# Kernel optimization log

Hardware: AMD Instinct MI355X
Metric: run time of the kernel (lower is better)

## Reference

```python
import jax, jax.numpy as jnp
import numpy as np

N = 50000
E = 800000
IN_C = 128
HEADS = 2
OUT_C = 64
NEG_SLOPE = 0.2  # PyG GATConv leaky_relu slope


def setup_inputs() -> dict:
    key = jax.random.key(0)
    ks = jax.random.split(key, 12)
    glorot = lambda k, shape: jax.random.normal(k, shape, jnp.float32) * np.sqrt(2.0 / (shape[0] + shape[-1]))
    return {
        "node_h": jax.random.normal(ks[0], (N, IN_C), jnp.float32),
        "edge_index_pc": jax.random.randint(ks[1], (2, E), 0, N, jnp.int64),
        "edge_index_mc": jax.random.randint(ks[2], (2, E), 0, N, jnp.int64),
        "W_pc": glorot(ks[3], (IN_C, HEADS * OUT_C)),
        "att_src_pc": glorot(ks[4], (HEADS, OUT_C)),
        "att_dst_pc": glorot(ks[5], (HEADS, OUT_C)),
        "bias_pc": jnp.zeros((HEADS * OUT_C,), jnp.float32),
        "W_mc": glorot(ks[6], (IN_C, HEADS * OUT_C)),
        "att_src_mc": glorot(ks[7], (HEADS, OUT_C)),
        "att_dst_mc": glorot(ks[8], (HEADS, OUT_C)),
        "bias_mc": jnp.zeros((HEADS * OUT_C,), jnp.float32),
    }


def _gat_conv(x, edge_index, W, att_src, att_dst, bias):
    # PyG GATConv (concat=True). x: [N, in], edge_index: [2, E] (src -> dst).
    n = x.shape[0]
    H, C = att_src.shape
    xw = (x @ W).reshape(n, H, C)                      # [N, H, C]
    a_src = jnp.sum(xw * att_src, axis=-1)             # [N, H]
    a_dst = jnp.sum(xw * att_dst, axis=-1)             # [N, H]
    src, dst = edge_index[0], edge_index[1]
    e = jax.nn.leaky_relu(a_src[src] + a_dst[dst], negative_slope=NEG_SLOPE)  # [E, H]
    # segment softmax over edges sharing the same destination node
    m = jax.ops.segment_max(e, dst, num_segments=n)    # [N, H]
    m = jnp.where(jnp.isfinite(m), m, 0.0)             # guard isolated nodes
    ex = jnp.exp(e - m[dst])
    denom = jax.ops.segment_sum(ex, dst, num_segments=n)
    alpha = ex / (denom[dst] + 1e-16)                  # [E, H]
    msg = xw[src] * alpha[:, :, None]                  # [E, H, C]
    out = jax.ops.segment_sum(msg, dst, num_segments=n)  # [N, H, C]
    return out.reshape(n, H * C) + bias


def reference(node_h, edge_index_pc, edge_index_mc,
              W_pc, att_src_pc, att_dst_pc, bias_pc,
              W_mc, att_src_mc, att_dst_mc, bias_mc):
    # eval mode: F.dropout and GATConv attention dropout are identity
    h_pc = jax.nn.elu(_gat_conv(node_h, edge_index_pc, W_pc, att_src_pc, att_dst_pc, bias_pc))
    h_mc = jax.nn.elu(_gat_conv(node_h, edge_index_mc, W_mc, att_src_mc, att_dst_mc, bias_mc))
    return (h_pc + h_mc) * 0.5
```

## Files before the change

### kernel.cpp

```cpp
#include <hip/hip_runtime.h>
#include <hip/hip_bf16.h>

#define IN_C   128
#define HC     128
#define OUT_C  64
#define EPB    4096
#define NBMAX  1024
#define CAP    4096

typedef short bf16x8 __attribute__((ext_vector_type(8)));
typedef float f32x4  __attribute__((ext_vector_type(4)));

__device__ __forceinline__ unsigned short f2bf(float f) {
    unsigned u = __float_as_uint(f);
    return (unsigned short)((u + 0x7FFF + ((u >> 16) & 1)) >> 16);
}

__device__ __forceinline__ void fma8(float* acc, float al, uint4 v) {
    acc[0] += al * __uint_as_float(v.x << 16);
    acc[1] += al * __uint_as_float(v.x & 0xFFFF0000u);
    acc[2] += al * __uint_as_float(v.y << 16);
    acc[3] += al * __uint_as_float(v.y & 0xFFFF0000u);
    acc[4] += al * __uint_as_float(v.z << 16);
    acc[5] += al * __uint_as_float(v.z & 0xFFFF0000u);
    acc[6] += al * __uint_as_float(v.w << 16);
    acc[7] += al * __uint_as_float(v.w & 0xFFFF0000u);
}

__global__ void k_detect(const void* __restrict__ h,
                         const void* __restrict__ e1,
                         const void* __restrict__ e2,
                         int* __restrict__ flags)
{
    if (blockIdx.x == 0 && threadIdx.x == 0) {
        const unsigned short* u = (const unsigned short*)h;
        int f32 = 0;
        for (int k = 0; k < 512; ++k) {
            int ex = (u[k] >> 7) & 0xFF;
            if (ex >= 0xE0) { f32 = 1; break; }
        }
        flags[0] = f32;
        const int* a = (const int*)e1;
        const int* b = (const int*)e2;
        int any1 = 0, any2 = 0;
        for (int k = 0; k < 64; ++k) { any1 |= a[2*k+1]; any2 |= b[2*k+1]; }
        flags[1] = (any1 == 0);
        flags[2] = (any2 == 0);
        flags[3] = 0;
    }
}

__device__ __forceinline__ float ldf(const void* p, int i, int f32) {
    if (f32) return ((const float*)p)[i];
    return __bfloat162float(((const __hip_bfloat16*)p)[i]);
}

__device__ __forceinline__ void load_edge(const void* ei, int e, int E, int i64,
                                          int& s, int& d)
{
    if (i64) {
        s = (int)((const long long*)ei)[e];
        d = (int)((const long long*)ei)[E + e];
    } else {
        s = ((const int*)ei)[e];
        d = ((const int*)ei)[E + e];
    }
}

__global__ void k_fill_sentinel(float* out, int total, float v)
{
    int i = blockIdx.x * blockDim.x + threadIdx.x;
    if (i < total) out[i] = v;
}

__global__ __launch_bounds__(256)
void k_prep(const void* __restrict__ Wpc, const void* __restrict__ Wmc,
            const int* __restrict__ flags,
            unsigned short* __restrict__ WTpc, unsigned short* __restrict__ WTmc)
{
    int idx = blockIdx.x * 256 + threadIdx.x;
    if (idx >= 2 * IN_C * HC) return;
    int conv = idx >= IN_C * HC;
    int r = idx - conv * IN_C * HC;
    int k = r >> 7, j = r & 127;
    float v = ldf(conv ? Wmc : Wpc, r, flags[0]);
    (conv ? WTmc : WTpc)[(size_t)j * IN_C + k] = f2bf(v);
}

__global__ __launch_bounds__(256)
void k_gs(const void* __restrict__ h,
          const unsigned short* __restrict__ WT0,
          const unsigned short* __restrict__ WT1,
          const void* __restrict__ atS0, const void* __restrict__ atD0,
          const void* __restrict__ atS1, const void* __restrict__ atD1,
          const int* __restrict__ flags,
          unsigned short* __restrict__ xw0, unsigned short* __restrict__ xw1,
          float* __restrict__ oas0, float* __restrict__ oad0,
          float* __restrict__ oas1, float* __restrict__ oad1,
          int n, int blocksG,
          const void* __restrict__ e1, const void* __restrict__ e2, int E,
          int NB, int blocksB,
          int* __restrict__ gcur1, int* __restrict__ gcur2,
          unsigned* __restrict__ bkt1, unsigned* __restrict__ bkt2)
{
    __shared__ int sh[2 * NBMAX];
    int tid = threadIdx.x;

    if (blockIdx.y < 2) {
        if ((int)blockIdx.x >= blocksG) return;
        int conv = blockIdx.y;
        const unsigned short* WT = conv ? WT1 : WT0;
        const void* atS = conv ? atS1 : atS0;
        const void* atD = conv ? atD1 : atD0;
        unsigned short* xw = conv ? xw1 : xw0;
        float* oaS = conv ? oas1 : oas0;
        float* oaD = conv ? oad1 : oad0;

        int wave = tid >> 6, lane = tid & 63;
        int cl = lane & 15, grp = lane >> 4;
        int base = blockIdx.x * 64 + wave * 16;
        int f32 = flags[0];

        int nodeLoad = base + cl;
        int nl = nodeLoad < n ? nodeLoad : (n - 1);
        bf16x8 afr[4];
        #pragma unroll
        for (int s = 0; s < 4; ++s) {
            int k0 = 32 * s + 8 * grp;
            if (f32) {
                const float4* hr = (const float4*)((const float*)h + (size_t)nl * IN_C + k0);
                float4 u0 = hr[0], u1 = hr[1];
                afr[s][0] = (short)f2bf(u0.x); afr[s][1] = (short)f2bf(u0.y);
                afr[s][2] = (short)f2bf(u0.z); afr[s][3] = (short)f2bf(u0.w);
                afr[s][4] = (short)f2bf(u1.x); afr[s][5] = (short)f2bf(u1.y);
                afr[s][6] = (short)f2bf(u1.z); afr[s][7] = (short)f2bf(u1.w);
            } else {
                afr[s] = *(const bf16x8*)((const unsigned short*)h + (size_t)nl * IN_C + k0);
            }
        }

        float vs_[4][2] = {{0.f,0.f},{0.f,0.f},{0.f,0.f},{0.f,0.f}};
        float vd_[4][2] = {{0.f,0.f},{0.f,0.f},{0.f,0.f},{0.f,0.f}};

        #pragma unroll
        for (int t = 0; t < 8; ++t) {
            int col = t * 16 + cl;
            f32x4 acc = {0.f, 0.f, 0.f, 0.f};
            #pragma unroll
            for (int s = 0; s < 4; ++s) {
                int k0 = 32 * s + 8 * grp;
                bf16x8 b = *(const bf16x8*)(WT + (size_t)col * IN_C + k0);
                acc = __builtin_amdgcn_mfma_f32_16x16x32_bf16(afr[s], b, acc, 0, 0, 0);
            }
            float aS = ldf(atS, col, f32);
            float aD = ldf(atD, col, f32);
            int hd = t >> 2;
            #pragma unroll
            for (int r = 0; r < 4; ++r) {
                int nodeOut = base + 4 * grp + r;
                float v = acc[r];
                if (nodeOut < n) xw[(size_t)nodeOut * HC + col] = f2bf(v);
                vs_[r][hd] += v * aS;
                vd_[r][hd] += v * aD;
            }
        }
        #pragma unroll
        for (int r = 0; r < 4; ++r) {
            #pragma unroll
            for (int hd = 0; hd < 2; ++hd) {
                float vs = vs_[r][hd], vd = vd_[r][hd];
                #pragma unroll
                for (int off = 1; off < 16; off <<= 1) {
                    vs += __shfl_xor(vs, off);
                    vd += __shfl_xor(vd, off);
                }
                int nodeOut = base + 4 * grp + r;
                if (cl == 0 && nodeOut < n) {
                    oaS[nodeOut * 2 + hd] = vs;
                    oaD[nodeOut * 2 + hd] = vd;
                }
            }
        }
    } else {
        if ((int)blockIdx.x >= blocksB) return;
        int conv = blockIdx.y - 2;
        const void* ei = conv ? e2 : e1;
        int* gcur = conv ? gcur2 : gcur1;
        unsigned* bkt = conv ? bkt2 : bkt1;
        int* cnt = sh;
        int* lbase = sh + NBMAX;
        for (int i = tid; i < NB; i += 256) cnt[i] = 0;
        __syncthreads();
        int base = blockIdx.x * EPB;
        int i64 = flags[1 + conv];
        int ss[EPB / 256], dd[EPB / 256];
        #pragma unroll
        for (int k = 0; k < EPB / 256; ++k) {
            int e = base + k * 256 + tid;
            if (e < E) {
                int s, d; load_edge(ei, e, E, i64, s, d);
                ss[k] = s; dd[k] = d;
                atomicAdd(&cnt[d >> 7], 1);
            } else dd[k] = -1;
        }
        __syncthreads();
        for (int i = tid; i < NB; i += 256) {
            int c = cnt[i];
            lbase[i] = c ? atomicAdd(&gcur[i], c) : 0;
            cnt[i] = 0;
        }
        __syncthreads();
        #pragma unroll
        for (int k = 0; k < EPB / 256; ++k) {
            if (dd[k] >= 0) {
                int b = dd[k] >> 7;
                int pos = lbase[b] + atomicAdd(&cnt[b], 1);
                if (pos < CAP)
                    bkt[(size_t)b * CAP + pos] =
                        ((unsigned)(dd[k] & 127) << 17) | (unsigned)ss[k];
            }
        }
    }
}

__global__ __launch_bounds__(256)
void k_bcsr3(unsigned* __restrict__ bkt1, unsigned* __restrict__ bkt2,
             const int* __restrict__ gcur1, const int* __restrict__ gcur2,
             int2* __restrict__ rs1, int2* __restrict__ rs2,
             int NB, int n)
{
    __shared__ unsigned ebuf[CAP];
    __shared__ int cnt[128], off[128], exc[128];
    int conv = blockIdx.y;
    unsigned* seg = (conv ? bkt2 : bkt1) + (size_t)blockIdx.x * CAP;
    const int* gcur = conv ? gcur2 : gcur1;
    int2* rs = conv ? rs2 : rs1;
    int b = blockIdx.x, tid = threadIdx.x;
    int nb0 = b << 7;
    int nd = n - nb0; if (nd > 128) nd = 128;
    int cntE = gcur[b]; if (cntE > CAP) cntE = CAP;

    for (int i = tid; i < cntE; i += 256) ebuf[i] = seg[i];
    if (tid < 128) cnt[tid] = 0;
    __syncthreads();
    for (int i = tid; i < cntE; i += 256)
        atomicAdd(&cnt[ebuf[i] >> 17], 1);
    __syncthreads();
    int v = (tid < 128) ? cnt[tid] : 0;
    if (tid < 128) off[tid] = v;
    __syncthreads();
    for (int o = 1; o < 128; o <<= 1) {
        int x = (tid < 128 && tid >= o) ? off[tid - o] : 0;
        __syncthreads();
        if (tid < 128) off[tid] += x;
        __syncthreads();
    }
    if (tid < 128) exc[tid] = off[tid] - v;
    if (tid < nd) {
        int begA = b * CAP + exc[tid];
        rs[nb0 + tid] = make_int2(begA, begA + v);
    }
    if (tid < 128) cnt[tid] = 0;
    __syncthreads();
    for (int i = tid; i < cntE; i += 256) {
        unsigned pv = ebuf[i];
        int d = pv >> 17;
        int pos = atomicAdd(&cnt[d], 1);
        seg[exc[d] + pos] = pv & 0x1FFFFu;
    }
}

__global__ __launch_bounds__(256)
void k_node8(const int2* __restrict__ rs1, const int2* __restrict__ rs2,
             const unsigned* __restrict__ csr1, const unsigned* __restrict__ csr2,
             const float* __restrict__ as1, const float* __restrict__ ad1,
             const float* __restrict__ as2, const float* __restrict__ ad2,
             const unsigned short* __restrict__ xw1, const unsigned short* __restrict__ xw2,
             const void* __restrict__ bias1, const void* __restrict__ bias2,
             const int* __restrict__ flags,
             float* __restrict__ out, int n)
{
    __shared__ int   slds[16][66];
    __shared__ float e0l[16][66];
    __shared__ float e1l[16][66];
    int tid = threadIdx.x;
    int nl = tid >> 4;
    int l  = tid & 15;
    int node = blockIdx.x * 16 + nl;
    if (node >= n) return;
    int f32 = flags[0];
    unsigned lofs = (unsigned)(l << 4);
    int c0 = l * 8;
    float vv0[8];

    #pragma unroll
    for (int conv = 0; conv < 2; ++conv) {
        const int2* rs = conv ? rs2 : rs1;
        const unsigned* csr = conv ? csr2 : csr1;
        const float2* asv = (const float2*)(conv ? as2 : as1);
        const float2* adv = (const float2*)(conv ? ad2 : ad1);
        const char* xwb = (const char*)(conv ? xw2 : xw1);
        const void* bias = conv ? bias2 : bias1;

        int2 r = rs[node];
        int beg = r.x, end = r.y;
        int deg = end - beg;
        float2 ad = adv[node];

        float m0 = -1e30f, m1 = -1e30f;
        for (int f = l; f < deg; f += 16) {
            int src = (int)csr[beg + f];
            float2 as = asv[src];
            float e0 = as.x + ad.x; e0 = e0 > 0.f ? e0 : 0.2f * e0;
            float e1 = as.y + ad.y; e1 = e1 > 0.f ? e1 : 0.2f * e1;
            if (f < 64) { slds[nl][f] = src; e0l[nl][f] = e0; e1l[nl][f] = e1; }
            m0 = fmaxf(m0, e0); m1 = fmaxf(m1, e1);
        }
        #pragma unroll
        for (int off = 8; off; off >>= 1) {
            m0 = fmaxf(m0, __shfl_xor(m0, off));
            m1 = fmaxf(m1, __shfl_xor(m1, off));
        }

        float s0 = 0.f, s1 = 0.f;
        for (int f = l; f < deg; f += 16) {
            float ex0, ex1;
            if (f < 64) {
                ex0 = expf(e0l[nl][f] - m0);
                ex1 = expf(e1l[nl][f] - m1);
                e0l[nl][f] = ex0; e1l[nl][f] = ex1;
            } else {
                int src = (int)csr[beg + f];
                float2 as = asv[src];
                float e0 = as.x + ad.x; e0 = e0 > 0.f ? e0 : 0.2f * e0;
                float e1 = as.y + ad.y; e1 = e1 > 0.f ? e1 : 0.2f * e1;
                ex0 = expf(e0 - m0); ex1 = expf(e1 - m1);
            }
            s0 += ex0; s1 += ex1;
        }
        #pragma unroll
        for (int off = 8; off; off >>= 1) {
            s0 += __shfl_xor(s0, off);
            s1 += __shfl_xor(s1, off);
        }
        float inv = (l < 8) ? 1.f / (s0 + 1e-16f) : 1.f / (s1 + 1e-16f);
        float mh  = (l < 8) ? m0 : m1;

        float acc[8] = {0.f,0.f,0.f,0.f,0.f,0.f,0.f,0.f};
        int tcap = deg < 64 ? deg : 64;
        int t = 0;
        for (; t + 8 <= tcap; t += 8) {
            int s_[8]; float a_[8];
            #pragma unroll
            for (int u = 0; u < 8; ++u) {
                s_[u] = slds[nl][t + u];
                a_[u] = ((l < 8) ? e0l[nl][t + u] : e1l[nl][t + u]) * inv;
            }
            uint4 v0 = *(const uint4*)(xwb + (((unsigned)s_[0]) << 8) + lofs);
            uint4 v1 = *(const uint4*)(xwb + (((unsigned)s_[1]) << 8) + lofs);
            uint4 v2 = *(const uint4*)(xwb + (((unsigned)s_[2]) << 8) + lofs);
            uint4 v3 = *(const uint4*)(xwb + (((unsigned)s_[3]) << 8) + lofs);
            uint4 v4 = *(const uint4*)(xwb + (((unsigned)s_[4]) << 8) + lofs);
            uint4 v5 = *(const uint4*)(xwb + (((unsigned)s_[5]) << 8) + lofs);
            uint4 v6 = *(const uint4*)(xwb + (((unsigned)s_[6]) << 8) + lofs);
            uint4 v7 = *(const uint4*)(xwb + (((unsigned)s_[7]) << 8) + lofs);
            fma8(acc, a_[0], v0); fma8(acc, a_[1], v1);
            fma8(acc, a_[2], v2); fma8(acc, a_[3], v3);
            fma8(acc, a_[4], v4); fma8(acc, a_[5], v5);
            fma8(acc, a_[6], v6); fma8(acc, a_[7], v7);
        }
        for (; t + 4 <= tcap; t += 4) {
            int sA = slds[nl][t],   sB = slds[nl][t+1];
            int sC = slds[nl][t+2], sD = slds[nl][t+3];
            float aA = ((l < 8) ? e0l[nl][t]   : e1l[nl][t])   * inv;
            float aB = ((l < 8) ? e0l[nl][t+1] : e1l[nl][t+1]) * inv;
            float aC = ((l < 8) ? e0l[nl][t+2] : e1l[nl][t+2]) * inv;
            float aD = ((l < 8) ? e0l[nl][t+3] : e1l[nl][t+3]) * inv;
            uint4 vA = *(const uint4*)(xwb + (((unsigned)sA) << 8) + lofs);
            uint4 vB = *(const uint4*)(xwb + (((unsigned)sB) << 8) + lofs);
            uint4 vC = *(const uint4*)(xwb + (((unsigned)sC) << 8) + lofs);
            uint4 vD = *(const uint4*)(xwb + (((unsigned)sD) << 8) + lofs);
            fma8(acc, aA, vA);
            fma8(acc, aB, vB);
            fma8(acc, aC, vC);
            fma8(acc, aD, vD);
        }
        for (; t < tcap; ++t) {
            int src = slds[nl][t];
            float exv = ((l < 8) ? e0l[nl][t] : e1l[nl][t]) * inv;
            uint4 v = *(const uint4*)(xwb + (((unsigned)src) << 8) + lofs);
            fma8(acc, exv, v);
        }
        for (; t < deg; ++t) {
            int src = (int)csr[beg + t];
            float2 as = asv[src];
            float e = (l < 8) ? (as.x + ad.x) : (as.y + ad.y);
            e = e > 0.f ? e : 0.2f * e;
            float exv = expf(e - mh);
            uint4 v = *(const uint4*)(xwb + (((unsigned)src) << 8) + lofs);
            fma8(acc, exv * inv, v);
        }

        if (conv == 0) {
            #pragma unroll
            for (int j = 0; j < 8; ++j) {
                float v = acc[j] + ldf(bias, c0 + j, f32);
                vv0[j] = v > 0.f ? v : expf(v) - 1.f;
            }
        } else {
            float vv1[8];
            #pragma unroll
            for (int j = 0; j < 8; ++j) {
                float v = acc[j] + ldf(bias, c0 + j, f32);
                vv1[j] = v > 0.f ? v : expf(v) - 1.f;
            }
            float4* o4 = (float4*)(out + (size_t)node * HC + c0);
            o4[0] = make_float4(0.5f * (vv0[0] + vv1[0]), 0.5f * (vv0[1] + vv1[1]),
                                0.5f * (vv0[2] + vv1[2]), 0.5f * (vv0[3] + vv1[3]));
            o4[1] = make_float4(0.5f * (vv0[4] + vv1[4]), 0.5f * (vv0[5] + vv1[5]),
                                0.5f * (vv0[6] + vv1[6]), 0.5f * (vv0[7] + vv1[7]));
        }
    }
}

static inline char* align64(char* p) {
    return (char*)(((size_t)p + 63) & ~(size_t)63);
}

extern "C" void kernel_launch(void* const* d_in, const int* in_sizes, int n_in,
                              void* d_out, int out_size, void* d_ws, size_t ws_size,
                              hipStream_t stream)
{
    const void* node_h = d_in[0];
    const void* ei_pc  = d_in[1];
    const void* ei_mc  = d_in[2];
    const void* W_pc   = d_in[3];
    const void* as_pc  = d_in[4];
    const void* ad_pc  = d_in[5];
    const void* b_pc   = d_in[6];
    const void* W_mc   = d_in[7];
    const void* as_mc  = d_in[8];
    const void* ad_mc  = d_in[9];
    const void* b_mc   = d_in[10];

    const int N = in_sizes[0] / IN_C;
    const int E = in_sizes[1] / 2;
    const int total = N * HC;
    const int NB = (N + 127) >> 7;
    float* out = (float*)d_out;
    const int fillBlocks = (out_size + 255) / 256;

    char* p = (char*)d_ws;
    int* flags = (int*)p;                       p += 256;
    unsigned short* WT_pc = (unsigned short*)p; p += (size_t)IN_C * HC * 2;
    unsigned short* WT_mc = (unsigned short*)p; p += (size_t)IN_C * HC * 2;
    unsigned short* xw_pc = (unsigned short*)p; p += (size_t)total * 2;
    unsigned short* xw_mc = (unsigned short*)p; p += (size_t)total * 2;
    float* aspc = (float*)p;                    p += (size_t)N * 2 * 4;
    float* adpc = (float*)p;                    p += (size_t)N * 2 * 4;
    float* asmc = (float*)p;                    p += (size_t)N * 2 * 4;
    float* admc = (float*)p;                    p += (size_t)N * 2 * 4;
    char* zbase = p;
    int* gcur1 = (int*)p;                       p += (size_t)NBMAX * 4;
    int* gcur2 = (int*)p;                       p += (size_t)NBMAX * 4;
    size_t zbytes = (size_t)(p - zbase);
    p = align64(p);
    int2* rs1 = (int2*)p;                       p += (size_t)N * 8;  p = align64(p);
    int2* rs2 = (int2*)p;                       p += (size_t)N * 8;  p = align64(p);
    unsigned* bkt1 = (unsigned*)p;              p += (size_t)NB * CAP * 4;
    unsigned* bkt2 = (unsigned*)p;              p += (size_t)NB * CAP * 4;

    {
        float sentinel = 0.f;
        if (n_in < 11) sentinel = 690.f;
        else if (in_sizes[1] != in_sizes[2]) sentinel = 702.f;
        else if (in_sizes[3] != IN_C * HC)   sentinel = 703.f;
        else if (in_sizes[7] != IN_C * HC)   sentinel = 707.f;
        else if (out_size != total)          sentinel = 720.f;
        else if (NB > NBMAX)                 sentinel = 730.f;
        else if (N >= (1 << 17))             sentinel = 741.f;
        size_t need = (size_t)(p - (char*)d_ws);
        if (sentinel == 0.f && ws_size < need) sentinel = 555.f;
        if (sentinel != 0.f) {
            k_fill_sentinel<<<fillBlocks, 256, 0, stream>>>(out, out_size, sentinel);
            return;
        }
    }

    k_detect<<<1, 64, 0, stream>>>(node_h, ei_pc, ei_mc, flags);
    k_prep<<<(2 * IN_C * HC + 255) / 256, 256, 0, stream>>>(W_pc, W_mc, flags, WT_pc, WT_mc);
    hipMemsetAsync(zbase, 0, zbytes, stream);

    const int blocksB = (E + EPB - 1) / EPB;
    const int blocksN = (N + 15) / 16;
    const int blocksG = (N + 63) / 64;
    const int gx = blocksG > blocksB ? blocksG : blocksB;

    k_gs<<<dim3(gx, 4), 256, 0, stream>>>(node_h, WT_pc, WT_mc,
                                          as_pc, ad_pc, as_mc, ad_mc, flags,
                                          xw_pc, xw_mc, aspc, adpc, asmc, admc,
                                          N, blocksG,
                                          ei_pc, ei_mc, E, NB, blocksB,
                                          gcur1, gcur2, bkt1, bkt2);

    k_bcsr3<<<dim3(NB, 2), 256, 0, stream>>>(bkt1, bkt2, gcur1, gcur2, rs1, rs2, NB, N);

    k_node8<<<blocksN, 256, 0, stream>>>(rs1, rs2, bkt1, bkt2,
                                         aspc, adpc, asmc, admc,
                                         xw_pc, xw_mc, b_pc, b_mc, flags,
                                         out, N);
}
```

Before: 149.6 us.

## Split the two GAT convolutions across sibling 16-lane groups per node

The node kernel now assigns each node to two adjacent 16-lane groups, one per convolution, instead of one group running both convolutions in sequence. Each group computes its own softmax and aggregation, and the results are combined through a cross-lane shuffle before a single store. This doubles the parallelism and memory-level concurrency per node and halves the nodes per block, at the cost of twice as many blocks. The 8-wide unrolled gather loop is removed, leaving the 4-wide loop as the widest, which lowers register pressure but also reduces loads in flight per thread. Early return when node>=n sits before the shuffle, but both groups of a node exit together, so the pairing stays consistent.

```diff
diff --git a/kernel.cpp b/kernel.cpp
--- a/kernel.cpp
+++ b/kernel.cpp
@@ -271,155 +271,129 @@
 }
 
 __global__ __launch_bounds__(256)
-void k_node8(const int2* __restrict__ rs1, const int2* __restrict__ rs2,
-             const unsigned* __restrict__ csr1, const unsigned* __restrict__ csr2,
-             const float* __restrict__ as1, const float* __restrict__ ad1,
-             const float* __restrict__ as2, const float* __restrict__ ad2,
-             const unsigned short* __restrict__ xw1, const unsigned short* __restrict__ xw2,
-             const void* __restrict__ bias1, const void* __restrict__ bias2,
-             const int* __restrict__ flags,
-             float* __restrict__ out, int n)
+void k_node10(const int2* __restrict__ rs1, const int2* __restrict__ rs2,
+              const unsigned* __restrict__ csr1, const unsigned* __restrict__ csr2,
+              const float* __restrict__ as1, const float* __restrict__ ad1,
+              const float* __restrict__ as2, const float* __restrict__ ad2,
+              const unsigned short* __restrict__ xw1, const unsigned short* __restrict__ xw2,
+              const void* __restrict__ bias1, const void* __restrict__ bias2,
+              const int* __restrict__ flags,
+              float* __restrict__ out, int n)
 {
     __shared__ int   slds[16][66];
     __shared__ float e0l[16][66];
     __shared__ float e1l[16][66];
     int tid = threadIdx.x;
-    int nl = tid >> 4;
+    int sl = tid >> 4;
     int l  = tid & 15;
-    int node = blockIdx.x * 16 + nl;
+    int conv = sl & 1;
+    int node = blockIdx.x * 8 + (sl >> 1);
     if (node >= n) return;
     int f32 = flags[0];
     unsigned lofs = (unsigned)(l << 4);
     int c0 = l * 8;
-    float vv0[8];
-
+
+    const int2* rs = conv ? rs2 : rs1;
+    const unsigned* csr = conv ? csr2 : csr1;
+    const float2* asv = (const float2*)(conv ? as2 : as1);
+    const float2* adv = (const float2*)(conv ? ad2 : ad1);
+    const char* xwb = (const char*)(conv ? xw2 : xw1);
+    const void* bias = conv ? bias2 : bias1;
+
+    int2 r = rs[node];
+    int beg = r.x, end = r.y;
+    int deg = end - beg;
+    float2 ad = adv[node];
+
+    float m0 = -1e30f, m1 = -1e30f;
+    for (int f = l; f < deg; f += 16) {
+        int src = (int)csr[beg + f];
+        float2 as = asv[src];
+        float e0 = as.x + ad.x; e0 = e0 > 0.f ? e0 : 0.2f * e0;
+        float e1 = as.y + ad.y; e1 = e1 > 0.f ? e1 : 0.2f * e1;
+        if (f < 64) { slds[sl][f] = src; e0l[sl][f] = e0; e1l[sl][f] = e1; }
+        m0 = fmaxf(m0, e0); m1 = fmaxf(m1, e1);
+    }
     #pragma unroll
-    for (int conv = 0; conv < 2; ++conv) {
-        const int2* rs = conv ? rs2 : rs1;
-        const unsigned* csr = conv ? csr2 : csr1;
-        const float2* asv = (const float2*)(conv ? as2 : as1);
-        const float2* adv = (const float2*)(conv ? ad2 : ad1);
-        const char* xwb = (const char*)(conv ? xw2 : xw1);
-        const void* bias = conv ? bias2 : bias1;
-
-        int2 r = rs[node];
-        int beg = r.x, end = r.y;
-        int deg = end - beg;
-        float2 ad = adv[node];
-
-        float m0 = -1e30f, m1 = -1e30f;
-        for (int f = l; f < deg; f += 16) {
+    for (int off = 8; off; off >>= 1) {
+        m0 = fmaxf(m0, __shfl_xor(m0, off));
+        m1 = fmaxf(m1, __shfl_xor(m1, off));
+    }
+
+    float s0 = 0.f, s1 = 0.f;
+    for (int f = l; f < deg; f += 16) {
+        float ex0, ex1;
+        if (f < 64) {
+            ex0 = expf(e0l[sl][f] - m0);
+            ex1 = expf(e1l[sl][f] - m1);
+            e0l[sl][f] = ex0; e1l[sl][f] = ex1;
+        } else {
             int src = (int)csr[beg + f];
             float2 as = asv[src];
             float e0 = as.x + ad.x; e0 = e0 > 0.f ? e0 : 0.2f * e0;
             float e1 = as.y + ad.y; e1 = e1 > 0.f ? e1 : 0.2f * e1;
-            if (f < 64) { slds[nl][f] = src; e0l[nl][f] = e0; e1l[nl][f] = e1; }
-            m0 = fmaxf(m0, e0); m1 = fmaxf(m1, e1);
-        }
-        #pragma unroll
-        for (int off = 8; off; off >>= 1) {
-            m0 = fmaxf(m0, __shfl_xor(m0, off));
-            m1 = fmaxf(m1, __shfl_xor(m1, off));
-        }
-
-        float s0 = 0.f, s1 = 0.f;
-        for (int f = l; f < deg; f += 16) {
-            float ex0, ex1;
-            if (f < 64) {
-                ex0 = expf(e0l[nl][f] - m0);
-                ex1 = expf(e1l[nl][f] - m1);
-                e0l[nl][f] = ex0; e1l[nl][f] = ex1;
-            } else {
-                int src = (int)csr[beg + f];
-                float2 as = asv[src];
-                float e0 = as.x + ad.x; e0 = e0 > 0.f ? e0 : 0.2f * e0;
-                float e1 = as.y + ad.y; e1 = e1 > 0.f ? e1 : 0.2f * e1;
-                ex0 = expf(e0 - m0); ex1 = expf(e1 - m1);
-            }
-            s0 += ex0; s1 += ex1;
-        }
-        #pragma unroll
-        for (int off = 8; off; off >>= 1) {
-            s0 += __shfl_xor(s0, off);
-            s1 += __shfl_xor(s1, off);
-        }
-        float inv = (l < 8) ? 1.f / (s0 + 1e-16f) : 1.f / (s1 + 1e-16f);
-        float mh  = (l < 8) ? m0 : m1;
-
-        float acc[8] = {0.f,0.f,0.f,0.f,0.f,0.f,0.f,0.f};
-        int tcap = deg < 64 ? deg : 64;
-        int t = 0;
-        for (; t + 8 <= tcap; t += 8) {
-            int s_[8]; float a_[8];
-            #pragma unroll
-            for (int u = 0; u < 8; ++u) {
-                s_[u] = slds[nl][t + u];
-                a_[u] = ((l < 8) ? e0l[nl][t + u] : e1l[nl][t + u]) * inv;
-            }
-            uint4 v0 = *(const uint4*)(xwb + (((unsigned)s_[0]) << 8) + lofs);
-            uint4 v1 = *(const uint4*)(xwb + (((unsigned)s_[1]) << 8) + lofs);
-            uint4 v2 = *(const uint4*)(xwb + (((unsigned)s_[2]) << 8) + lofs);
-            uint4 v3 = *(const uint4*)(xwb + (((unsigned)s_[3]) << 8) + lofs);
-            uint4 v4 = *(const uint4*)(xwb + (((unsigned)s_[4]) << 8) + lofs);
-            uint4 v5 = *(const uint4*)(xwb + (((unsigned)s_[5]) << 8) + lofs);
-            uint4 v6 = *(const uint4*)(xwb + (((unsigned)s_[6]) << 8) + lofs);
-            uint4 v7 = *(const uint4*)(xwb + (((unsigned)s_[7]) << 8) + lofs);
-            fma8(acc, a_[0], v0); fma8(acc, a_[1], v1);
-            fma8(acc, a_[2], v2); fma8(acc, a_[3], v3);
-            fma8(acc, a_[4], v4); fma8(acc, a_[5], v5);
-            fma8(acc, a_[6], v6); fma8(acc, a_[7], v7);
-        }
-        for (; t + 4 <= tcap; t += 4) {
-            int sA = slds[nl][t],   sB = slds[nl][t+1];
-            int sC = slds[nl][t+2], sD = slds[nl][t+3];
-            float aA = ((l < 8) ? e0l[nl][t]   : e1l[nl][t])   * inv;
-            float aB = ((l < 8) ? e0l[nl][t+1] : e1l[nl][t+1]) * inv;
-            float aC = ((l < 8) ? e0l[nl][t+2] : e1l[nl][t+2]) * inv;
-            float aD = ((l < 8) ? e0l[nl][t+3] : e1l[nl][t+3]) * inv;
-            uint4 vA = *(const uint4*)(xwb + (((unsigned)sA) << 8) + lofs);
-            uint4 vB = *(const uint4*)(xwb + (((unsigned)sB) << 8) + lofs);
-            uint4 vC = *(const uint4*)(xwb + (((unsigned)sC) << 8) + lofs);
-            uint4 vD = *(const uint4*)(xwb + (((unsigned)sD) << 8) + lofs);
-            fma8(acc, aA, vA);
-            fma8(acc, aB, vB);
-            fma8(acc, aC, vC);
-            fma8(acc, aD, vD);
-        }
-        for (; t < tcap; ++t) {
-            int src = slds[nl][t];
-            float exv = ((l < 8) ? e0l[nl][t] : e1l[nl][t]) * inv;
-            uint4 v = *(const uint4*)(xwb + (((unsigned)src) << 8) + lofs);
-            fma8(acc, exv, v);
-        }
-        for (; t < deg; ++t) {
-            int src = (int)csr[beg + t];
-            float2 as = asv[src];
-            float e = (l < 8) ? (as.x + ad.x) : (as.y + ad.y);
-            e = e > 0.f ? e : 0.2f * e;
-            float exv = expf(e - mh);
-            uint4 v = *(const uint4*)(xwb + (((unsigned)src) << 8) + lofs);
-            fma8(acc, exv * inv, v);
-        }
-
-        if (conv == 0) {
-            #pragma unroll
-            for (int j = 0; j < 8; ++j) {
-                float v = acc[j] + ldf(bias, c0 + j, f32);
-                vv0[j] = v > 0.f ? v : expf(v) - 1.f;
-            }
-        } else {
-            float vv1[8];
-            #pragma unroll
-            for (int j = 0; j < 8; ++j) {
-                float v = acc[j] + ldf(bias, c0 + j, f32);
-                vv1[j] = v > 0.f ? v : expf(v) - 1.f;
-            }
-            float4* o4 = (float4*)(out + (size_t)node * HC + c0);
-            o4[0] = make_float4(0.5f * (vv0[0] + vv1[0]), 0.5f * (vv0[1] + vv1[1]),
-                                0.5f * (vv0[2] + vv1[2]), 0.5f * (vv0[3] + vv1[3]));
-            o4[1] = make_float4(0.5f * (vv0[4] + vv1[4]), 0.5f * (vv0[5] + vv1[5]),
-                                0.5f * (vv0[6] + vv1[6]), 0.5f * (vv0[7] + vv1[7]));
-        }
+            ex0 = expf(e0 - m0); ex1 = expf(e1 - m1);
+        }
+        s0 += ex0; s1 += ex1;
+    }
+    #pragma unroll
+    for (int off = 8; off; off >>= 1) {
+        s0 += __shfl_xor(s0, off);
+        s1 += __shfl_xor(s1, off);
+    }
+    float inv = (l < 8) ? 1.f / (s0 + 1e-16f) : 1.f / (s1 + 1e-16f);
+    float mh  = (l < 8) ? m0 : m1;
+
+    float acc[8] = {0.f,0.f,0.f,0.f,0.f,0.f,0.f,0.f};
+    int tcap = deg < 64 ? deg : 64;
+    int t = 0;
+    for (; t + 4 <= tcap; t += 4) {
+        int sA = slds[sl][t],   sB = slds[sl][t+1];
+        int sC = slds[sl][t+2], sD = slds[sl][t+3];
+        float aA = ((l < 8) ? e0l[sl][t]   : e1l[sl][t])   * inv;
+        float aB = ((l < 8) ? e0l[sl][t+1] : e1l[sl][t+1]) * inv;
+        float aC = ((l < 8) ? e0l[sl][t+2] : e1l[sl][t+2]) * inv;
+        float aD = ((l < 8) ? e0l[sl][t+3] : e1l[sl][t+3]) * inv;
+        uint4 vA = *(const uint4*)(xwb + (((unsigned)sA) << 8) + lofs);
+        uint4 vB = *(const uint4*)(xwb + (((unsigned)sB) << 8) + lofs);
+        uint4 vC = *(const uint4*)(xwb + (((unsigned)sC) << 8) + lofs);
+        uint4 vD = *(const uint4*)(xwb + (((unsigned)sD) << 8) + lofs);
+        fma8(acc, aA, vA);
+        fma8(acc, aB, vB);
+        fma8(acc, aC, vC);
+        fma8(acc, aD, vD);
+    }
+    for (; t < tcap; ++t) {
+        int src = slds[sl][t];
+        float exv = ((l < 8) ? e0l[sl][t] : e1l[sl][t]) * inv;
+        uint4 v = *(const uint4*)(xwb + (((unsigned)src) << 8) + lofs);
+        fma8(acc, exv, v);
+    }
+    for (; t < deg; ++t) {
+        int src = (int)csr[beg + t];
+        float2 as = asv[src];
+        float e = (l < 8) ? (as.x + ad.x) : (as.y + ad.y);
+        e = e > 0.f ? e : 0.2f * e;
+        float exv = expf(e - mh);
+        uint4 v = *(const uint4*)(xwb + (((unsigned)src) << 8) + lofs);
+        fma8(acc, exv * inv, v);
+    }
+
+    float vv[8];
+    #pragma unroll
+    for (int j = 0; j < 8; ++j) {
+        float v = acc[j] + ldf(bias, c0 + j, f32);
+        vv[j] = v > 0.f ? v : expf(v) - 1.f;
+    }
+    float ov[8];
+    #pragma unroll
+    for (int j = 0; j < 8; ++j) ov[j] = __shfl_xor(vv[j], 16);
+    if (conv == 0) {
+        float4* o4 = (float4*)(out + (size_t)node * HC + c0);
+        o4[0] = make_float4(0.5f * (vv[0] + ov[0]), 0.5f * (vv[1] + ov[1]),
+                            0.5f * (vv[2] + ov[2]), 0.5f * (vv[3] + ov[3]));
+        o4[1] = make_float4(0.5f * (vv[4] + ov[4]), 0.5f * (vv[5] + ov[5]),
+                            0.5f * (vv[6] + ov[6]), 0.5f * (vv[7] + ov[7]));
     }
 }
 
@@ -492,7 +466,7 @@
     hipMemsetAsync(zbase, 0, zbytes, stream);
 
     const int blocksB = (E + EPB - 1) / EPB;
-    const int blocksN = (N + 15) / 16;
+    const int blocksN = (N + 7) / 8;
     const int blocksG = (N + 63) / 64;
     const int gx = blocksG > blocksB ? blocksG : blocksB;
 
@@ -505,8 +479,8 @@
 
     k_bcsr3<<<dim3(NB, 2), 256, 0, stream>>>(bkt1, bkt2, gcur1, gcur2, rs1, rs2, NB, N);
 
-    k_node8<<<blocksN, 256, 0, stream>>>(rs1, rs2, bkt1, bkt2,
-                                         aspc, adpc, asmc, admc,
-                                         xw_pc, xw_mc, b_pc, b_mc, flags,
-                                         out, N);
-}
+    k_node10<<<blocksN, 256, 0, stream>>>(rs1, rs2, bkt1, bkt2,
+                                          aspc, adpc, asmc, admc,
+                                          xw_pc, xw_mc, b_pc, b_mc, flags,
+                                          out, N);
+}
```

Measured after the change: 150.7 us. About the same (+0.8%).

## Move segment softmax into CSR build kernel, store bf16 alphas per edge

Applied to the files above, without the earlier changes.

Attention logits, max, exp and normalisation now run inside the bucket CSR-build kernel, using shared memory per 128-node bucket. Each edge's alpha pair is written as packed bf16 next to its source index, so the node aggregation kernel only gathers xw rows and applies the precomputed weights. This removes the redundant a_src gathers and exp work from the node kernel, and its shared-memory staging. In exchange it adds an extra per-edge global array, quantises alpha to bf16, and cuts bucket capacity to 3072 to fit the larger LDS footprint, which risks truncating heavily loaded buckets.

```diff
diff --git a/kernel.cpp b/kernel.cpp
--- a/kernel.cpp
+++ b/kernel.cpp
@@ -6,7 +6,7 @@
 #define OUT_C  64
 #define EPB    4096
 #define NBMAX  1024
-#define CAP    4096
+#define CAP    3072
 
 typedef short bf16x8 __attribute__((ext_vector_type(8)));
 typedef float f32x4  __attribute__((ext_vector_type(4)));
@@ -224,16 +224,24 @@
 }
 
 __global__ __launch_bounds__(256)
-void k_bcsr3(unsigned* __restrict__ bkt1, unsigned* __restrict__ bkt2,
+void k_bcsr4(unsigned* __restrict__ bkt1, unsigned* __restrict__ bkt2,
+             unsigned* __restrict__ alp1, unsigned* __restrict__ alp2,
              const int* __restrict__ gcur1, const int* __restrict__ gcur2,
+             const float* __restrict__ as1, const float* __restrict__ ad1,
+             const float* __restrict__ as2, const float* __restrict__ ad2,
              int2* __restrict__ rs1, int2* __restrict__ rs2,
              int NB, int n)
 {
     __shared__ unsigned ebuf[CAP];
+    __shared__ float sc0[CAP];
+    __shared__ float sc1[CAP];
     __shared__ int cnt[128], off[128], exc[128];
     int conv = blockIdx.y;
     unsigned* seg = (conv ? bkt2 : bkt1) + (size_t)blockIdx.x * CAP;
+    unsigned* alp = (conv ? alp2 : alp1) + (size_t)blockIdx.x * CAP;
     const int* gcur = conv ? gcur2 : gcur1;
+    const float2* asv = (const float2*)(conv ? as2 : as1);
+    const float2* adv = (const float2*)(conv ? ad2 : ad1);
     int2* rs = conv ? rs2 : rs1;
     int b = blockIdx.x, tid = threadIdx.x;
     int nb0 = b << 7;
@@ -268,21 +276,49 @@
         int pos = atomicAdd(&cnt[d], 1);
         seg[exc[d] + pos] = pv & 0x1FFFFu;
     }
+    __syncthreads();
+
+    int d = tid >> 1, sub = tid & 1;
+    int rc = (d < nd) ? cnt[d] : 0;
+    int rb = exc[d];
+    float2 ad = (d < nd) ? adv[nb0 + d] : make_float2(0.f, 0.f);
+    float m0 = -1e30f, m1 = -1e30f;
+    for (int i = sub; i < rc; i += 2) {
+        int s = (int)seg[rb + i];
+        float2 as = asv[s];
+        float e0 = as.x + ad.x; e0 = e0 > 0.f ? e0 : 0.2f * e0;
+        float e1 = as.y + ad.y; e1 = e1 > 0.f ? e1 : 0.2f * e1;
+        sc0[rb + i] = e0; sc1[rb + i] = e1;
+        m0 = fmaxf(m0, e0); m1 = fmaxf(m1, e1);
+    }
+    m0 = fmaxf(m0, __shfl_xor(m0, 1));
+    m1 = fmaxf(m1, __shfl_xor(m1, 1));
+    float s0 = 0.f, s1 = 0.f;
+    for (int i = sub; i < rc; i += 2) {
+        float ex0 = expf(sc0[rb + i] - m0);
+        float ex1 = expf(sc1[rb + i] - m1);
+        sc0[rb + i] = ex0; sc1[rb + i] = ex1;
+        s0 += ex0; s1 += ex1;
+    }
+    s0 += __shfl_xor(s0, 1);
+    s1 += __shfl_xor(s1, 1);
+    float inv0 = 1.f / (s0 + 1e-16f), inv1 = 1.f / (s1 + 1e-16f);
+    for (int i = sub; i < rc; i += 2) {
+        unsigned a = (unsigned)f2bf(sc0[rb + i] * inv0)
+                   | ((unsigned)f2bf(sc1[rb + i] * inv1) << 16);
+        alp[rb + i] = a;
+    }
 }
 
 __global__ __launch_bounds__(256)
-void k_node8(const int2* __restrict__ rs1, const int2* __restrict__ rs2,
-             const unsigned* __restrict__ csr1, const unsigned* __restrict__ csr2,
-             const float* __restrict__ as1, const float* __restrict__ ad1,
-             const float* __restrict__ as2, const float* __restrict__ ad2,
-             const unsigned short* __restrict__ xw1, const unsigned short* __restrict__ xw2,
-             const void* __restrict__ bias1, const void* __restrict__ bias2,
-             const int* __restrict__ flags,
-             float* __restrict__ out, int n)
-{
-    __shared__ int   slds[16][66];
-    __shared__ float e0l[16][66];
-    __shared__ float e1l[16][66];
+void k_node11(const int2* __restrict__ rs1, const int2* __restrict__ rs2,
+              const unsigned* __restrict__ csr1, const unsigned* __restrict__ csr2,
+              const unsigned* __restrict__ alp1, const unsigned* __restrict__ alp2,
+              const unsigned short* __restrict__ xw1, const unsigned short* __restrict__ xw2,
+              const void* __restrict__ bias1, const void* __restrict__ bias2,
+              const int* __restrict__ flags,
+              float* __restrict__ out, int n)
+{
     int tid = threadIdx.x;
     int nl = tid >> 4;
     int l  = tid & 15;
@@ -291,114 +327,46 @@
     int f32 = flags[0];
     unsigned lofs = (unsigned)(l << 4);
     int c0 = l * 8;
+    int hi = (l >= 8);
     float vv0[8];
 
     #pragma unroll
     for (int conv = 0; conv < 2; ++conv) {
         const int2* rs = conv ? rs2 : rs1;
         const unsigned* csr = conv ? csr2 : csr1;
-        const float2* asv = (const float2*)(conv ? as2 : as1);
-        const float2* adv = (const float2*)(conv ? ad2 : ad1);
+        const unsigned* alp = conv ? alp2 : alp1;
         const char* xwb = (const char*)(conv ? xw2 : xw1);
         const void* bias = conv ? bias2 : bias1;
 
         int2 r = rs[node];
-        int beg = r.x, end = r.y;
-        int deg = end - beg;
-        float2 ad = adv[node];
-
-        float m0 = -1e30f, m1 = -1e30f;
-        for (int f = l; f < deg; f += 16) {
-            int src = (int)csr[beg + f];
-            float2 as = asv[src];
-            float e0 = as.x + ad.x; e0 = e0 > 0.f ? e0 : 0.2f * e0;
-            float e1 = as.y + ad.y; e1 = e1 > 0.f ? e1 : 0.2f * e1;
-            if (f < 64) { slds[nl][f] = src; e0l[nl][f] = e0; e1l[nl][f] = e1; }
-            m0 = fmaxf(m0, e0); m1 = fmaxf(m1, e1);
-        }
-        #pragma unroll
-        for (int off = 8; off; off >>= 1) {
-            m0 = fmaxf(m0, __shfl_xor(m0, off));
-            m1 = fmaxf(m1, __shfl_xor(m1, off));
-        }
-
-        float s0 = 0.f, s1 = 0.f;
-        for (int f = l; f < deg; f += 16) {
-            float ex0, ex1;
-            if (f < 64) {
-                ex0 = expf(e0l[nl][f] - m0);
-                ex1 = expf(e1l[nl][f] - m1);
-                e0l[nl][f] = ex0; e1l[nl][f] = ex1;
-            } else {
-                int src = (int)csr[beg + f];
-                float2 as = asv[src];
-                float e0 = as.x + ad.x; e0 = e0 > 0.f ? e0 : 0.2f * e0;
-                float e1 = as.y + ad.y; e1 = e1 > 0.f ? e1 : 0.2f * e1;
-                ex0 = expf(e0 - m0); ex1 = expf(e1 - m1);
-            }
-            s0 += ex0; s1 += ex1;
-        }
-        #pragma unroll
-        for (int off = 8; off; off >>= 1) {
-            s0 += __shfl_xor(s0, off);
-            s1 += __shfl_xor(s1, off);
-        }
-        float inv = (l < 8) ? 1.f / (s0 + 1e-16f) : 1.f / (s1 + 1e-16f);
-        float mh  = (l < 8) ? m0 : m1;
+        int beg = r.x, deg = r.y - r.x;
 
         float acc[8] = {0.f,0.f,0.f,0.f,0.f,0.f,0.f,0.f};
-        int tcap = deg < 64 ? deg : 64;
         int t = 0;
-        for (; t + 8 <= tcap; t += 8) {
-            int s_[8]; float a_[8];
-            #pragma unroll
-            for (int u = 0; u < 8; ++u) {
-                s_[u] = slds[nl][t + u];
-                a_[u] = ((l < 8) ? e0l[nl][t + u] : e1l[nl][t + u]) * inv;
-            }
-            uint4 v0 = *(const uint4*)(xwb + (((unsigned)s_[0]) << 8) + lofs);
-            uint4 v1 = *(const uint4*)(xwb + (((unsigned)s_[1]) << 8) + lofs);
-            uint4 v2 = *(const uint4*)(xwb + (((unsigned)s_[2]) << 8) + lofs);
-            uint4 v3 = *(const uint4*)(xwb + (((unsigned)s_[3]) << 8) + lofs);
-            uint4 v4 = *(const uint4*)(xwb + (((unsigned)s_[4]) << 8) + lofs);
-            uint4 v5 = *(const uint4*)(xwb + (((unsigned)s_[5]) << 8) + lofs);
-            uint4 v6 = *(const uint4*)(xwb + (((unsigned)s_[6]) << 8) + lofs);
-            uint4 v7 = *(const uint4*)(xwb + (((unsigned)s_[7]) << 8) + lofs);
-            fma8(acc, a_[0], v0); fma8(acc, a_[1], v1);
-            fma8(acc, a_[2], v2); fma8(acc, a_[3], v3);
-            fma8(acc, a_[4], v4); fma8(acc, a_[5], v5);
-            fma8(acc, a_[6], v6); fma8(acc, a_[7], v7);
-        }
-        for (; t + 4 <= tcap; t += 4) {
-            int sA = slds[nl][t],   sB = slds[nl][t+1];
-            int sC = slds[nl][t+2], sD = slds[nl][t+3];
-            float aA = ((l < 8) ? e0l[nl][t]   : e1l[nl][t])   * inv;
-            float aB = ((l < 8) ? e0l[nl][t+1] : e1l[nl][t+1]) * inv;
-            float aC = ((l < 8) ? e0l[nl][t+2] : e1l[nl][t+2]) * inv;
-            float aD = ((l < 8) ? e0l[nl][t+3] : e1l[nl][t+3]) * inv;
-            uint4 vA = *(const uint4*)(xwb + (((unsigned)sA) << 8) + lofs);
-            uint4 vB = *(const uint4*)(xwb + (((unsigned)sB) << 8) + lofs);
-            uint4 vC = *(const uint4*)(xwb + (((unsigned)sC) << 8) + lofs);
-            uint4 vD = *(const uint4*)(xwb + (((unsigned)sD) << 8) + lofs);
-            fma8(acc, aA, vA);
-            fma8(acc, aB, vB);
-            fma8(acc, aC, vC);
-            fma8(acc, aD, vD);
-        }
-        for (; t < tcap; ++t) {
-            int src = slds[nl][t];
-            float exv = ((l < 8) ? e0l[nl][t] : e1l[nl][t]) * inv;
-            uint4 v = *(const uint4*)(xwb + (((unsigned)src) << 8) + lofs);
-            fma8(acc, exv, v);
+        for (; t + 4 <= deg; t += 4) {
+            unsigned sA = csr[beg + t],     sB = csr[beg + t + 1];
+            unsigned sC = csr[beg + t + 2], sD = csr[beg + t + 3];
+            unsigned aA = alp[beg + t],     aB = alp[beg + t + 1];
+            unsigned aC = alp[beg + t + 2], aD = alp[beg + t + 3];
+            uint4 vA = *(const uint4*)(xwb + (sA << 8) + lofs);
+            uint4 vB = *(const uint4*)(xwb + (sB << 8) + lofs);
+            uint4 vC = *(const uint4*)(xwb + (sC << 8) + lofs);
+            uint4 vD = *(const uint4*)(xwb + (sD << 8) + lofs);
+            float alA = __uint_as_float(hi ? (aA & 0xFFFF0000u) : (aA << 16));
+            float alB = __uint_as_float(hi ? (aB & 0xFFFF0000u) : (aB << 16));
+            float alC = __uint_as_float(hi ? (aC & 0xFFFF0000u) : (aC << 16));
+            float alD = __uint_as_float(hi ? (aD & 0xFFFF0000u) : (aD << 16));
+            fma8(acc, alA, vA);
+            fma8(acc, alB, vB);
+            fma8(acc, alC, vC);
+            fma8(acc, alD, vD);
         }
         for (; t < deg; ++t) {
-            int src = (int)csr[beg + t];
-            float2 as = asv[src];
-            float e = (l < 8) ? (as.x + ad.x) : (as.y + ad.y);
-            e = e > 0.f ? e : 0.2f * e;
-            float exv = expf(e - mh);
-            uint4 v = *(const uint4*)(xwb + (((unsigned)src) << 8) + lofs);
-            fma8(acc, exv * inv, v);
+            unsigned s = csr[beg + t];
+            unsigned a = alp[beg + t];
+            float al = __uint_as_float(hi ? (a & 0xFFFF0000u) : (a << 16));
+            uint4 v = *(const uint4*)(xwb + (s << 8) + lofs);
+            fma8(acc, al, v);
         }
 
         if (conv == 0) {
@@ -469,6 +437,8 @@
     int2* rs2 = (int2*)p;                       p += (size_t)N * 8;  p = align64(p);
     unsigned* bkt1 = (unsigned*)p;              p += (size_t)NB * CAP * 4;
     unsigned* bkt2 = (unsigned*)p;              p += (size_t)NB * CAP * 4;
+    unsigned* alp1 = (unsigned*)p;              p += (size_t)NB * CAP * 4;
+    unsigned* alp2 = (unsigned*)p;              p += (size_t)NB * CAP * 4;
 
     {
         float sentinel = 0.f;
@@ -503,10 +473,12 @@
                                           ei_pc, ei_mc, E, NB, blocksB,
                                           gcur1, gcur2, bkt1, bkt2);
 
-    k_bcsr3<<<dim3(NB, 2), 256, 0, stream>>>(bkt1, bkt2, gcur1, gcur2, rs1, rs2, NB, N);
-
-    k_node8<<<blocksN, 256, 0, stream>>>(rs1, rs2, bkt1, bkt2,
-                                         aspc, adpc, asmc, admc,
-                                         xw_pc, xw_mc, b_pc, b_mc, flags,
-                                         out, N);
-}
+    k_bcsr4<<<dim3(NB, 2), 256, 0, stream>>>(bkt1, bkt2, alp1, alp2,
+                                             gcur1, gcur2,
+                                             aspc, adpc, asmc, admc,
+                                             rs1, rs2, NB, N);
+
+    k_node11<<<blocksN, 256, 0, stream>>>(rs1, rs2, bkt1, bkt2, alp1, alp2,
+                                          xw_pc, xw_mc, b_pc, b_mc, flags,
+                                          out, N);
+}
```

New measurement: 154.4 us. +3.2%, slower.
